# Kernel optimization log

Measured on AMD Instinct MI355X. Metric: run time of the kernel, lower is better.

## Reference

```python
import jax, jax.numpy as jnp
import numpy as np
from jax import lax

N_CHANNELS = 64
N_FILTERS = 256
N_LAYERS = 9  # residual blocks use dilations 2**1 .. 2**(N_LAYERS-1)


def causal_conv1d(x, w, dilation):
    """Causal dilated conv. x: [B,T,Cin], w: [K,Cin,Cout]."""
    pad = (w.shape[0] - 1) * dilation
    return lax.conv_general_dilated(
        x, w, window_strides=(1,), padding=[(pad, 0)],
        rhs_dilation=(dilation,), dimension_numbers=("NWC", "WIO", "NWC"))


def setup_inputs() -> dict:
    key = jax.random.key(0)
    ks = jax.random.split(key, 12)
    B, T, C, F, L = 8, 4096, N_CHANNELS, N_FILTERS, N_LAYERS
    s = lambda fan_in: 1.0 / np.sqrt(fan_in)
    return {
        "x": jax.random.normal(ks[0], (B, T, C), jnp.float32),
        "Wc": jax.random.normal(ks[1], (2, C, F), jnp.float32) * s(2 * C),
        "Wf": jax.random.normal(ks[2], (L - 1, 2, F, F), jnp.float32) * s(2 * F),
        "Wg": jax.random.normal(ks[3], (L - 1, 2, F, F), jnp.float32) * s(2 * F),
        "Wr": jax.random.normal(ks[4], (L - 1, F, F), jnp.float32) * s(F),
        "br": jnp.zeros((L - 1, F), jnp.float32),
        "Ws": jax.random.normal(ks[5], (L - 1, F, F), jnp.float32) * s(F),
        "bs": jnp.zeros((L - 1, F), jnp.float32),
        "Wd1": jax.random.normal(ks[6], (F, C), jnp.float32) * s(F),
        "bd1": jnp.zeros((C,), jnp.float32),
        "Wd2": jax.random.normal(ks[7], (C, C), jnp.float32) * s(C),
        "bd2": jnp.zeros((C,), jnp.float32),
    }


def reference(x, Wc, Wf, Wg, Wr, br, Ws, bs, Wd1, bd1, Wd2, bd2):
    # Initial causal conv, dilation 1, no bias.
    out = causal_conv1d(x, Wc, 1)  # [B,T,F]
    skip_sum = jnp.zeros_like(out)
    for i in range(N_LAYERS - 1):
        d = 2 ** (i + 1)
        f = causal_conv1d(out, Wf[i], d)
        g = causal_conv1d(out, Wg[i], d)
        z = jnp.tanh(f) * jax.nn.sigmoid(g)
        out = out + jnp.einsum("btf,fo->bto", z, Wr[i]) + br[i]
        skip_sum = skip_sum + jnp.einsum("btf,fo->bto", z, Ws[i]) + bs[i]
    h = jax.nn.selu(skip_sum)
    h = jnp.einsum("btf,fc->btc", h, Wd1) + bd1
    h = jax.nn.selu(h)
    h = jnp.einsum("btc,co->bto", h, Wd2) + bd2
    return h
```

## Files before the change

### kernel.cpp

```cpp
#include <hip/hip_runtime.h>
#include <cstdint>

typedef unsigned short u16;
typedef unsigned int u32;
typedef __attribute__((ext_vector_type(8))) short s8v;
typedef __attribute__((ext_vector_type(4))) float f4v;

#define FCH 256

__device__ __forceinline__ float bf2f(u16 u){ return __uint_as_float(((u32)u)<<16); }
__device__ __forceinline__ u16 f2bf(float x){
  u32 u = __float_as_uint(x);
  u += 0x7fffu + ((u>>16)&1u);
  return (u16)(u>>16);
}
__device__ __forceinline__ uint4 pack8(float4 a, float4 b){
  uint4 o;
  o.x = (u32)f2bf(a.x) | ((u32)f2bf(a.y)<<16);
  o.y = (u32)f2bf(a.z) | ((u32)f2bf(a.w)<<16);
  o.z = (u32)f2bf(b.x) | ((u32)f2bf(b.y)<<16);
  o.w = (u32)f2bf(b.z) | ((u32)f2bf(b.w)<<16);
  return o;
}
__device__ __forceinline__ float seluf(float x){
  const float sc = 1.0507009873554805f, al = 1.6732632423543772f;
  return x > 0.f ? sc*x : sc*al*(__expf(x)-1.f);
}
__device__ __forceinline__ int xcd_tile(int bid, int nT8){
  return nT8 ? ((bid & 7) * nT8 + (bid >> 3)) : bid;
}

__global__ __launch_bounds__(256) void pack_kernel(
    const float* __restrict__ Wc, const float* __restrict__ Wf, const float* __restrict__ Wg,
    const float* __restrict__ Wr, const float* __restrict__ Ws,
    const float* __restrict__ Wd1, const float* __restrict__ Wd2,
    u16* __restrict__ Bp1, u16* __restrict__ Bp2, u16* __restrict__ Bp0,
    u16* __restrict__ BpD1, u16* __restrict__ BpD2)
{
  int gid = blockIdx.x*256 + threadIdx.x;
  int frag = gid >> 6;
  int lane = gid & 63;
  int q = lane >> 4, i15 = lane & 15;
  u16 v[8];
  u16* dst;
  if (frag < 4096) {
    int layer = frag >> 9, rem = frag & 511;
    int kc = rem >> 5, nt = rem & 31;
    int n = nt*16 + i15;
    const float* W = (n < 256) ? Wf : Wg;
    int nn = (n < 256) ? n : n - 256;
    #pragma unroll
    for (int j = 0; j < 8; ++j) {
      int k = kc*32 + q*8 + j;
      int tap = k >> 8, cin = k & 255;
      v[j] = f2bf(W[((size_t)((layer*2 + tap)*256 + cin))*256 + nn]);
    }
    dst = Bp1 + (size_t)frag*512 + lane*8;
  } else if (frag < 6144) {
    int f = frag - 4096;
    int layer = f >> 8, rem = f & 255;
    int kc = rem >> 5, nt = rem & 31;
    int n = nt*16 + i15;
    const float* W = (n < 256) ? Wr : Ws;
    int nn = (n < 256) ? n : n - 256;
    #pragma unroll
    for (int j = 0; j < 8; ++j) {
      int k = kc*32 + q*8 + j;
      v[j] = f2bf(W[((size_t)(layer*256 + k))*256 + nn]);
    }
    dst = Bp2 + (size_t)f*512 + lane*8;
  } else if (frag < 6208) {
    int f = frag - 6144;
    int kc = f >> 4, nt = f & 15;
    int n = nt*16 + i15;
    #pragma unroll
    for (int j = 0; j < 8; ++j) {
      int k = kc*32 + q*8 + j;
      int tap = k >> 6, cin = k & 63;
      v[j] = f2bf(Wc[(size_t)(tap*64 + cin)*256 + n]);
    }
    dst = Bp0 + (size_t)f*512 + lane*8;
  } else if (frag < 6240) {
    int f = frag - 6208;
    int kc = f >> 2, nt = f & 3;
    int n = nt*16 + i15;
    #pragma unroll
    for (int j = 0; j < 8; ++j) {
      int k = kc*32 + q*8 + j;
      v[j] = f2bf(Wd1[(size_t)k*64 + n]);
    }
    dst = BpD1 + (size_t)f*512 + lane*8;
  } else if (frag < 6248) {
    int f = frag - 6240;
    int kc = f >> 2, nt = f & 3;
    int n = nt*16 + i15;
    #pragma unroll
    for (int j = 0; j < 8; ++j) {
      int k = kc*32 + q*8 + j;
      v[j] = f2bf(Wd2[(size_t)k*64 + n]);
    }
    dst = BpD2 + (size_t)f*512 + lane*8;
  } else return;
  uint4 o;
  o.x = (u32)v[0] | ((u32)v[1] << 16);
  o.y = (u32)v[2] | ((u32)v[3] << 16);
  o.z = (u32)v[4] | ((u32)v[5] << 16);
  o.w = (u32)v[6] | ((u32)v[7] << 16);
  *reinterpret_cast<uint4*>(dst) = o;
}

__global__ __launch_bounds__(256, 2) void conv0_kernel(
    const float* __restrict__ x, u16* __restrict__ outBf,
    const u16* __restrict__ Bp0, int nT8)
{
  __shared__ __align__(16) u16 ldsA[2][2048];
  const int tid = threadIdx.x;
  const int w = tid >> 6, lane = tid & 63, q = lane >> 4, i15 = lane & 15;
  const int rb = xcd_tile(blockIdx.x, nT8) * 64;
  const int sm = tid >> 2, sg = tid & 3;
  const int grow = rb + sm;
  const int tpos = grow & 4095;
  const int sunit = ((sm >> 4)*64 + sg*16 + ((sm & 15) ^ (sg << 1))) * 8;
  const int runit = (q*16 + (i15 ^ (q << 1))) * 8;

  f4v acc[4][4];
  #pragma unroll
  for (int jj = 0; jj < 4; ++jj)
    #pragma unroll
    for (int mt = 0; mt < 4; ++mt)
      acc[jj][mt] = (f4v){0.f,0.f,0.f,0.f};

  float4 f0 = {0.f,0.f,0.f,0.f}, f1 = {0.f,0.f,0.f,0.f};
  if (tpos >= 1) {
    const float* px = x + (size_t)(grow-1)*64 + sg*8;
    f0 = *reinterpret_cast<const float4*>(px);
    f1 = *reinterpret_cast<const float4*>(px + 4);
  }
  *reinterpret_cast<uint4*>(&ldsA[0][sunit]) = pack8(f0, f1);
  s8v bcur[4], bnxt[4];
  #pragma unroll
  for (int jj = 0; jj < 4; ++jj)
    bcur[jj] = *reinterpret_cast<const s8v*>(Bp0 + ((size_t)(w + 4*jj)*64 + lane)*8);
  __syncthreads();

  for (int kc = 0; kc < 4; ++kc) {
    const int cur = kc & 1;
    uint4 an = {0u,0u,0u,0u};
    if (kc < 3) {
      int kg = (kc+1)*32 + sg*8;
      int tap = kg >> 6, col = kg & 63;
      float4 g0 = {0.f,0.f,0.f,0.f}, g1 = {0.f,0.f,0.f,0.f};
      if (tap) {
        const float* px = x + (size_t)grow*64 + col;
        g0 = *reinterpret_cast<const float4*>(px);
        g1 = *reinterpret_cast<const float4*>(px + 4);
      } else if (tpos >= 1) {
        const float* px = x + (size_t)(grow-1)*64 + col;
        g0 = *reinterpret_cast<const float4*>(px);
        g1 = *reinterpret_cast<const float4*>(px + 4);
      }
      an = pack8(g0, g1);
      #pragma unroll
      for (int jj = 0; jj < 4; ++jj)
        bnxt[jj] = *reinterpret_cast<const s8v*>(Bp0 + (((size_t)(kc+1)*16 + (w + 4*jj))*64 + lane)*8);
    }
    s8v af[4];
    #pragma unroll
    for (int mt = 0; mt < 4; ++mt)
      af[mt] = *reinterpret_cast<const s8v*>(&ldsA[cur][mt*512 + runit]);
    #pragma unroll
    for (int jj = 0; jj < 4; ++jj)
      #pragma unroll
      for (int mt = 0; mt < 4; ++mt)
        acc[jj][mt] = __builtin_amdgcn_mfma_f32_16x16x32_bf16(af[mt], bcur[jj], acc[jj][mt], 0,0,0);
    if (kc < 3) {
      *reinterpret_cast<uint4*>(&ldsA[cur ^ 1][sunit]) = an;
      #pragma unroll
      for (int jj = 0; jj < 4; ++jj) bcur[jj] = bnxt[jj];
    }
    __syncthreads();
  }

  #pragma unroll
  for (int jj = 0; jj < 4; ++jj) {
    const int cc = (w + 4*jj)*16 + i15;
    #pragma unroll
    for (int mt = 0; mt < 4; ++mt)
      #pragma unroll
      for (int r = 0; r < 4; ++r) {
        const int g2 = rb + mt*16 + q*4 + r;
        outBf[(size_t)g2*FCH + cc] = f2bf(acc[jj][mt][r]);
      }
  }
}

__global__ __launch_bounds__(256, 3) void layer_kernel(
    const u16* __restrict__ inBf, u16* __restrict__ outBf,
    u16* __restrict__ skipB,
    const u16* __restrict__ Bp1, const u16* __restrict__ Bp2,
    const float* __restrict__ br, const float* __restrict__ bs,
    int dil, int first, int nT8)
{
  __shared__ __align__(16) u16 ldsA[2][32*40];
  __shared__ __align__(16) u16 ldsZ[32*264];
  const int tid = threadIdx.x;
  const int w = tid >> 6, lane = tid & 63, q = lane >> 4, i15 = lane & 15;
  const int rb = xcd_tile(blockIdx.x, nT8) * 32;
  const int sm = tid >> 3, sg = tid & 7;
  const int grow = rb + sm;
  const int tpos = grow & 4095;

  f4v acc[8][2];
  #pragma unroll
  for (int jj = 0; jj < 8; ++jj)
    #pragma unroll
    for (int mt = 0; mt < 2; ++mt)
      acc[jj][mt] = (f4v){0.f,0.f,0.f,0.f};

  {
    uint2 a0 = {0u,0u};
    if (tpos >= dil)
      a0 = *reinterpret_cast<const uint2*>(inBf + (size_t)(grow - dil)*FCH + sg*4);
    *reinterpret_cast<uint2*>(&ldsA[0][sm*40 + sg*4]) = a0;
    s8v bcur[8], bnxt[8];
    #pragma unroll
    for (int jj = 0; jj < 8; ++jj)
      bcur[jj] = *reinterpret_cast<const s8v*>(Bp1 + ((size_t)(w + 4*jj)*64 + lane)*8);
    __syncthreads();

    for (int kc = 0; kc < 16; ++kc) {
      const int cur = kc & 1;
      uint2 an = {0u,0u};
      if (kc < 15) {
        int kg = (kc+1)*32 + sg*4;
        int tap = kg >> 8, col = kg & 255;
        if (tap) an = *reinterpret_cast<const uint2*>(inBf + (size_t)grow*FCH + col);
        else if (tpos >= dil) an = *reinterpret_cast<const uint2*>(inBf + (size_t)(grow - dil)*FCH + col);
        #pragma unroll
        for (int jj = 0; jj < 8; ++jj)
          bnxt[jj] = *reinterpret_cast<const s8v*>(Bp1 + (((size_t)(kc+1)*32 + (w + 4*jj))*64 + lane)*8);
      }
      s8v af[2];
      #pragma unroll
      for (int mt = 0; mt < 2; ++mt)
        af[mt] = *reinterpret_cast<const s8v*>(&ldsA[cur][(mt*16 + i15)*40 + q*8]);
      #pragma unroll
      for (int jj = 0; jj < 8; ++jj)
        #pragma unroll
        for (int mt = 0; mt < 2; ++mt)
          acc[jj][mt] = __builtin_amdgcn_mfma_f32_16x16x32_bf16(af[mt], bcur[jj], acc[jj][mt], 0,0,0);
      if (kc < 15) {
        *reinterpret_cast<uint2*>(&ldsA[cur ^ 1][sm*40 + sg*4]) = an;
        #pragma unroll
        for (int jj = 0; jj < 8; ++jj) bcur[jj] = bnxt[jj];
      }
      __syncthreads();
    }
  }

  #pragma unroll
  for (int jj = 0; jj < 4; ++jj) {
    const int colb = (w + 4*jj)*16 + i15;
    #pragma unroll
    for (int mt = 0; mt < 2; ++mt)
      #pragma unroll
      for (int r = 0; r < 4; ++r) {
        float f = acc[jj][mt][r];
        float g = acc[jj+4][mt][r];
        float z = (1.f - 2.f/(__expf(2.f*f) + 1.f)) * (1.f/(1.f + __expf(-g)));
        ldsZ[(mt*16 + q*4 + r)*264 + colb] = f2bf(z);
      }
  }
  __syncthreads();

  #pragma unroll
  for (int jj = 0; jj < 8; ++jj) {
    const int nt = w + 4*jj;
    const bool isR = (jj < 4);
    const int cc = (isR ? nt*16 : (nt-16)*16) + i15;
    const float bias = isR ? br[cc] : bs[cc];
    #pragma unroll
    for (int mt = 0; mt < 2; ++mt)
      #pragma unroll
      for (int r = 0; r < 4; ++r) {
        const int g2 = rb + mt*16 + q*4 + r;
        float vv;
        if (isR) vv = bf2f(inBf[(size_t)g2*FCH + cc]) + bias;
        else     vv = first ? bias : (bf2f(skipB[(size_t)g2*FCH + cc]) + bias);
        acc[jj][mt][r] = vv;
      }
  }

  {
    s8v b2c[8], b2n[8];
    #pragma unroll
    for (int jj = 0; jj < 8; ++jj)
      b2c[jj] = *reinterpret_cast<const s8v*>(Bp2 + ((size_t)(w + 4*jj)*64 + lane)*8);
    for (int kc = 0; kc < 8; ++kc) {
      if (kc < 7) {
        #pragma unroll
        for (int jj = 0; jj < 8; ++jj)
          b2n[jj] = *reinterpret_cast<const s8v*>(Bp2 + (((size_t)(kc+1)*32 + (w + 4*jj))*64 + lane)*8);
      }
      s8v af[2];
      #pragma unroll
      for (int mt = 0; mt < 2; ++mt)
        af[mt] = *reinterpret_cast<const s8v*>(&ldsZ[(mt*16 + i15)*264 + kc*32 + q*8]);
      #pragma unroll
      for (int jj = 0; jj < 8; ++jj)
        #pragma unroll
        for (int mt = 0; mt < 2; ++mt)
          acc[jj][mt] = __builtin_amdgcn_mfma_f32_16x16x32_bf16(af[mt], b2c[jj], acc[jj][mt], 0,0,0);
      if (kc < 7) {
        #pragma unroll
        for (int jj = 0; jj < 8; ++jj) b2c[jj] = b2n[jj];
      }
    }
  }

  #pragma unroll
  for (int jj = 0; jj < 8; ++jj) {
    const int nt = w + 4*jj;
    const bool isR = (jj < 4);
    const int cc = (isR ? nt*16 : (nt-16)*16) + i15;
    #pragma unroll
    for (int mt = 0; mt < 2; ++mt)
      #pragma unroll
      for (int r = 0; r < 4; ++r) {
        const int g2 = rb + mt*16 + q*4 + r;
        u16 hv = f2bf(acc[jj][mt][r]);
        if (isR) outBf[(size_t)g2*FCH + cc] = hv;
        else     skipB[(size_t)g2*FCH + cc] = hv;
      }
  }
}

__global__ __launch_bounds__(256, 2) void final_kernel(
    const u16* __restrict__ skipB, const u16* __restrict__ BpD1, const u16* __restrict__ BpD2,
    const float* __restrict__ bd1, const float* __restrict__ bd2, float* __restrict__ outp,
    int nT8)
{
  __shared__ __align__(16) u16 ldsH[64*264];
  __shared__ __align__(16) u16 ldsH2[64*72];
  const int tid = threadIdx.x;
  const int w = tid >> 6, lane = tid & 63, q = lane >> 4, i15 = lane & 15;
  const int rb = xcd_tile(blockIdx.x, nT8) * 64;
  const int sm = tid >> 2, sseg = tid & 3;

  {
    const u16* sp = skipB + (size_t)(rb + sm)*256 + sseg*64;
    u16* dr = &ldsH[sm*264 + sseg*64];
    #pragma unroll
    for (int u = 0; u < 8; ++u) {
      uint4 raw = *reinterpret_cast<const uint4*>(sp + u*8);
      u32 rr[4] = {raw.x, raw.y, raw.z, raw.w};
      uint4 o;
      u32 oo[4];
      #pragma unroll
      for (int p = 0; p < 4; ++p) {
        float e0 = seluf(bf2f((u16)(rr[p] & 0xffffu)));
        float e1 = seluf(bf2f((u16)(rr[p] >> 16)));
        oo[p] = (u32)f2bf(e0) | ((u32)f2bf(e1) << 16);
      }
      o.x = oo[0]; o.y = oo[1]; o.z = oo[2]; o.w = oo[3];
      *reinterpret_cast<uint4*>(dr + u*8) = o;
    }
  }
  __syncthreads();

  f4v a1[4];
  #pragma unroll
  for (int mt = 0; mt < 4; ++mt) a1[mt] = (f4v){0.f,0.f,0.f,0.f};
  for (int kc = 0; kc < 8; ++kc) {
    s8v b = *reinterpret_cast<const s8v*>(BpD1 + ((size_t)(kc*4 + w)*64 + lane)*8);
    #pragma unroll
    for (int mt = 0; mt < 4; ++mt) {
      s8v af = *reinterpret_cast<const s8v*>(&ldsH[(mt*16 + i15)*264 + kc*32 + q*8]);
      a1[mt] = __builtin_amdgcn_mfma_f32_16x16x32_bf16(af, b, a1[mt], 0,0,0);
    }
  }
  const float bb1 = bd1[w*16 + i15];
  #pragma unroll
  for (int mt = 0; mt < 4; ++mt)
    #pragma unroll
    for (int r = 0; r < 4; ++r)
      ldsH2[(mt*16 + q*4 + r)*72 + w*16 + i15] = f2bf(seluf(a1[mt][r] + bb1));
  __syncthreads();

  f4v a2[4];
  #pragma unroll
  for (int mt = 0; mt < 4; ++mt) a2[mt] = (f4v){0.f,0.f,0.f,0.f};
  #pragma unroll
  for (int kc = 0; kc < 2; ++kc) {
    s8v b = *reinterpret_cast<const s8v*>(BpD2 + ((size_t)(kc*4 + w)*64 + lane)*8);
    #pragma unroll
    for (int mt = 0; mt < 4; ++mt) {
      s8v af = *reinterpret_cast<const s8v*>(&ldsH2[(mt*16 + i15)*72 + kc*32 + q*8]);
      a2[mt] = __builtin_amdgcn_mfma_f32_16x16x32_bf16(af, b, a2[mt], 0,0,0);
    }
  }
  const float bb2 = bd2[w*16 + i15];
  #pragma unroll
  for (int mt = 0; mt < 4; ++mt)
    #pragma unroll
    for (int r = 0; r < 4; ++r)
      outp[(size_t)(rb + mt*16 + q*4 + r)*64 + w*16 + i15] = a2[mt][r] + bb2;
}

__global__ __launch_bounds__(256) void zero_kernel(uint4* __restrict__ outp, int n16)
{
  int i = blockIdx.x*256 + threadIdx.x;
  if (i < n16) outp[i] = (uint4){0u,0u,0u,0u};
}

extern "C" void kernel_launch(void* const* d_in, const int* in_sizes, int n_in,
                              void* d_out, int out_size, void* d_ws, size_t ws_size,
                              hipStream_t stream)
{
  (void)n_in;
  const float* x   = (const float*)d_in[0];
  const float* Wc  = (const float*)d_in[1];
  const float* Wf  = (const float*)d_in[2];
  const float* Wg  = (const float*)d_in[3];
  const float* Wr  = (const float*)d_in[4];
  const float* br  = (const float*)d_in[5];
  const float* Ws  = (const float*)d_in[6];
  const float* bs  = (const float*)d_in[7];
  const float* Wd1 = (const float*)d_in[8];
  const float* bd1 = (const float*)d_in[9];
  const float* Wd2 = (const float*)d_in[10];
  const float* bd2 = (const float*)d_in[11];

  const size_t ROWS = (size_t)in_sizes[0] / 64;
  const int gridC = (int)(ROWS / 64);
  const int gridL = (int)(ROWS / 32);
  const int nT8C = (gridC % 8 == 0) ? gridC / 8 : 0;
  const int nT8L = (gridL % 8 == 0) ? gridL / 8 : 0;

  const size_t packsB = (size_t)6248 * 512 * 2;
  const size_t bfBuf  = ROWS * 256 * 2;
  const size_t needB = packsB + 3*bfBuf;

  if (ws_size < needB) {
    int n16 = (out_size * 4) / 16;
    zero_kernel<<<(n16 + 255)/256, 256, 0, stream>>>((uint4*)d_out, n16);
    return;
  }

  char* ws = (char*)d_ws;
  u16* Bp1    = (u16*)ws;            ws += (size_t)4096*512*2;
  u16* Bp2    = (u16*)ws;            ws += (size_t)2048*512*2;
  u16* Bp0    = (u16*)ws;            ws += (size_t)64*512*2;
  u16* BpD1   = (u16*)ws;            ws += (size_t)32*512*2;
  u16* BpD2   = (u16*)ws;            ws += (size_t)8*512*2;
  u16* skipB  = (u16*)ws;            ws += bfBuf;
  u16* bufA   = (u16*)ws;            ws += bfBuf;
  u16* bufB   = (u16*)ws;            ws += bfBuf;

  pack_kernel<<<1562, 256, 0, stream>>>(Wc, Wf, Wg, Wr, Ws, Wd1, Wd2,
                                        Bp1, Bp2, Bp0, BpD1, BpD2);
  conv0_kernel<<<gridC, 256, 0, stream>>>(x, bufA, Bp0, nT8C);
  u16* bufs[2] = {bufA, bufB};
  for (int i = 0; i < 8; ++i) {
    layer_kernel<<<gridL, 256, 0, stream>>>(
        bufs[i & 1], bufs[(i + 1) & 1], skipB,
        Bp1 + (size_t)i*262144, Bp2 + (size_t)i*131072,
        br + i*256, bs + i*256, 2 << i, (i == 0) ? 1 : 0, nT8L);
  }
  final_kernel<<<gridC, 256, 0, stream>>>(skipB, BpD1, BpD2, bd1, bd2,
                                          (float*)d_out, nT8C);
}
```

Before: 594.3 us.

## Load dilated-conv A fragments directly from global, drop LDS staging and barriers

The first GEMM in layer_kernel no longer stages the activation tile through double-buffered shared memory with a barrier every k-step. Each lane now reads its MFMA A fragment straight from global memory (the shifted tap first, then the current tap), and a zero fragment is used when the row is before the dilation. Both GEMM loops also drop the explicit register double-buffering of weight fragments and load each B fragment just before use, leaving the overlap to unroll-by-2 and the compiler. This removes the LDS traffic and per-step syncs and lowers register pressure, but the global A loads become less coalesced and B load latency may be less well hidden.

New measurement: 889.5 us. 49.7% more time.

```diff
diff --git a/kernel.cpp b/kernel.cpp
--- a/kernel.cpp
+++ b/kernel.cpp
@@ -201,14 +201,10 @@
     const float* __restrict__ br, const float* __restrict__ bs,
     int dil, int first, int nT8)
 {
-  __shared__ __align__(16) u16 ldsA[2][32*40];
   __shared__ __align__(16) u16 ldsZ[32*264];
   const int tid = threadIdx.x;
   const int w = tid >> 6, lane = tid & 63, q = lane >> 4, i15 = lane & 15;
   const int rb = xcd_tile(blockIdx.x, nT8) * 32;
-  const int sm = tid >> 3, sg = tid & 7;
-  const int grow = rb + sm;
-  const int tpos = grow & 4095;
 
   f4v acc[8][2];
   #pragma unroll
@@ -218,43 +214,45 @@
       acc[jj][mt] = (f4v){0.f,0.f,0.f,0.f};
 
   {
-    uint2 a0 = {0u,0u};
-    if (tpos >= dil)
-      a0 = *reinterpret_cast<const uint2*>(inBf + (size_t)(grow - dil)*FCH + sg*4);
-    *reinterpret_cast<uint2*>(&ldsA[0][sm*40 + sg*4]) = a0;
-    s8v bcur[8], bnxt[8];
-    #pragma unroll
-    for (int jj = 0; jj < 8; ++jj)
-      bcur[jj] = *reinterpret_cast<const s8v*>(Bp1 + ((size_t)(w + 4*jj)*64 + lane)*8);
-    __syncthreads();
-
-    for (int kc = 0; kc < 16; ++kc) {
-      const int cur = kc & 1;
-      uint2 an = {0u,0u};
-      if (kc < 15) {
-        int kg = (kc+1)*32 + sg*4;
-        int tap = kg >> 8, col = kg & 255;
-        if (tap) an = *reinterpret_cast<const uint2*>(inBf + (size_t)grow*FCH + col);
-        else if (tpos >= dil) an = *reinterpret_cast<const uint2*>(inBf + (size_t)(grow - dil)*FCH + col);
-        #pragma unroll
-        for (int jj = 0; jj < 8; ++jj)
-          bnxt[jj] = *reinterpret_cast<const s8v*>(Bp1 + (((size_t)(kc+1)*32 + (w + 4*jj))*64 + lane)*8);
-      }
+    const u16* aptr0[2];
+    const u16* aptr1[2];
+    bool vld[2];
+    #pragma unroll
+    for (int mt = 0; mt < 2; ++mt) {
+      const int row = rb + mt*16 + i15;
+      vld[mt]   = (row & 4095) >= dil;
+      aptr0[mt] = inBf + (size_t)(row - dil)*FCH + q*8;
+      aptr1[mt] = inBf + (size_t)row*FCH + q*8;
+    }
+    const s8v zz = {0,0,0,0,0,0,0,0};
+
+    #pragma unroll 2
+    for (int kc = 0; kc < 8; ++kc) {
       s8v af[2];
       #pragma unroll
       for (int mt = 0; mt < 2; ++mt)
-        af[mt] = *reinterpret_cast<const s8v*>(&ldsA[cur][(mt*16 + i15)*40 + q*8]);
-      #pragma unroll
-      for (int jj = 0; jj < 8; ++jj)
+        af[mt] = vld[mt] ? *reinterpret_cast<const s8v*>(aptr0[mt] + kc*32) : zz;
+      #pragma unroll
+      for (int jj = 0; jj < 8; ++jj) {
+        s8v b = *reinterpret_cast<const s8v*>(Bp1 + (((size_t)kc*32 + (w + 4*jj))*64 + lane)*8);
         #pragma unroll
         for (int mt = 0; mt < 2; ++mt)
-          acc[jj][mt] = __builtin_amdgcn_mfma_f32_16x16x32_bf16(af[mt], bcur[jj], acc[jj][mt], 0,0,0);
-      if (kc < 15) {
-        *reinterpret_cast<uint2*>(&ldsA[cur ^ 1][sm*40 + sg*4]) = an;
+          acc[jj][mt] = __builtin_amdgcn_mfma_f32_16x16x32_bf16(af[mt], b, acc[jj][mt], 0,0,0);
+      }
+    }
+    #pragma unroll 2
+    for (int kc = 8; kc < 16; ++kc) {
+      s8v af[2];
+      #pragma unroll
+      for (int mt = 0; mt < 2; ++mt)
+        af[mt] = *reinterpret_cast<const s8v*>(aptr1[mt] + (kc - 8)*32);
+      #pragma unroll
+      for (int jj = 0; jj < 8; ++jj) {
+        s8v b = *reinterpret_cast<const s8v*>(Bp1 + (((size_t)kc*32 + (w + 4*jj))*64 + lane)*8);
         #pragma unroll
-        for (int jj = 0; jj < 8; ++jj) bcur[jj] = bnxt[jj];
-      }
-      __syncthreads();
+        for (int mt = 0; mt < 2; ++mt)
+          acc[jj][mt] = __builtin_amdgcn_mfma_f32_16x16x32_bf16(af[mt], b, acc[jj][mt], 0,0,0);
+      }
     }
   }
 
@@ -292,28 +290,18 @@
   }
 
   {
-    s8v b2c[8], b2n[8];
-    #pragma unroll
-    for (int jj = 0; jj < 8; ++jj)
-      b2c[jj] = *reinterpret_cast<const s8v*>(Bp2 + ((size_t)(w + 4*jj)*64 + lane)*8);
+    #pragma unroll 2
     for (int kc = 0; kc < 8; ++kc) {
-      if (kc < 7) {
-        #pragma unroll
-        for (int jj = 0; jj < 8; ++jj)
-          b2n[jj] = *reinterpret_cast<const s8v*>(Bp2 + (((size_t)(kc+1)*32 + (w + 4*jj))*64 + lane)*8);
-      }
       s8v af[2];
       #pragma unroll
       for (int mt = 0; mt < 2; ++mt)
         af[mt] = *reinterpret_cast<const s8v*>(&ldsZ[(mt*16 + i15)*264 + kc*32 + q*8]);
       #pragma unroll
-      for (int jj = 0; jj < 8; ++jj)
+      for (int jj = 0; jj < 8; ++jj) {
+        s8v b = *reinterpret_cast<const s8v*>(Bp2 + (((size_t)kc*32 + (w + 4*jj))*64 + lane)*8);
         #pragma unroll
         for (int mt = 0; mt < 2; ++mt)
-          acc[jj][mt] = __builtin_amdgcn_mfma_f32_16x16x32_bf16(af[mt], b2c[jj], acc[jj][mt], 0,0,0);
-      if (kc < 7) {
-        #pragma unroll
-        for (int jj = 0; jj < 8; ++jj) b2c[jj] = b2n[jj];
+          acc[jj][mt] = __builtin_amdgcn_mfma_f32_16x16x32_bf16(af[mt], b, acc[jj][mt], 0,0,0);
       }
     }
   }
```

## Load dilated-conv A fragments directly from global memory and drop LDS staging

Applied to the files above, without the earlier changes.

The first GEMM in the layer kernel now loads each MFMA A fragment straight from global memory into registers, with a mask that zeroes causal-padding rows. This removes the double-buffered LDS tile and the per-k-step __syncthreads. The second GEMM prefetches its first B fragments and the next LDS Z fragments in software. The residual and skip loads are moved after the GEMM and added in the epilogue, with accumulators starting from zero. These changes cut barriers and LDS traffic, at the cost of redundant global loads across waves and more registers held live.

Measured after the change: 542.6 us. -8.7%, faster.

```diff
diff --git a/kernel.cpp b/kernel.cpp
--- a/kernel.cpp
+++ b/kernel.cpp
@@ -25,6 +25,12 @@
 __device__ __forceinline__ float seluf(float x){
   const float sc = 1.0507009873554805f, al = 1.6732632423543772f;
   return x > 0.f ? sc*x : sc*al*(__expf(x)-1.f);
+}
+__device__ __forceinline__ s8v ldmask(const u16* p, u32 m){
+  uint4 r = *reinterpret_cast<const uint4*>(p);
+  r.x &= m; r.y &= m; r.z &= m; r.w &= m;
+  s8v v; *reinterpret_cast<uint4*>(&v) = r;
+  return v;
 }
 __device__ __forceinline__ int xcd_tile(int bid, int nT8){
   return nT8 ? ((bid & 7) * nT8 + (bid >> 3)) : bid;
@@ -201,14 +207,10 @@
     const float* __restrict__ br, const float* __restrict__ bs,
     int dil, int first, int nT8)
 {
-  __shared__ __align__(16) u16 ldsA[2][32*40];
   __shared__ __align__(16) u16 ldsZ[32*264];
   const int tid = threadIdx.x;
   const int w = tid >> 6, lane = tid & 63, q = lane >> 4, i15 = lane & 15;
   const int rb = xcd_tile(blockIdx.x, nT8) * 32;
-  const int sm = tid >> 3, sg = tid & 7;
-  const int grow = rb + sm;
-  const int tpos = grow & 4095;
 
   f4v acc[8][2];
   #pragma unroll
@@ -218,45 +220,58 @@
       acc[jj][mt] = (f4v){0.f,0.f,0.f,0.f};
 
   {
-    uint2 a0 = {0u,0u};
-    if (tpos >= dil)
-      a0 = *reinterpret_cast<const uint2*>(inBf + (size_t)(grow - dil)*FCH + sg*4);
-    *reinterpret_cast<uint2*>(&ldsA[0][sm*40 + sg*4]) = a0;
-    s8v bcur[8], bnxt[8];
+    const u16* a0p[2];
+    const u16* a1p[2];
+    u32 am[2];
+    #pragma unroll
+    for (int mt = 0; mt < 2; ++mt) {
+      const int row = rb + mt*16 + i15;
+      const bool v = (row & 4095) >= dil;
+      a0p[mt] = inBf + (size_t)(v ? row - dil : row)*FCH + q*8;
+      a1p[mt] = inBf + (size_t)row*FCH + q*8;
+      am[mt]  = v ? 0xffffffffu : 0u;
+    }
+
+    s8v bcur[8], bnxt[8], afc[2], afn[2];
     #pragma unroll
     for (int jj = 0; jj < 8; ++jj)
       bcur[jj] = *reinterpret_cast<const s8v*>(Bp1 + ((size_t)(w + 4*jj)*64 + lane)*8);
-    __syncthreads();
-
+    #pragma unroll
+    for (int mt = 0; mt < 2; ++mt)
+      afc[mt] = ldmask(a0p[mt], am[mt]);
+
+    #pragma unroll 2
     for (int kc = 0; kc < 16; ++kc) {
-      const int cur = kc & 1;
-      uint2 an = {0u,0u};
-      if (kc < 15) {
-        int kg = (kc+1)*32 + sg*4;
-        int tap = kg >> 8, col = kg & 255;
-        if (tap) an = *reinterpret_cast<const uint2*>(inBf + (size_t)grow*FCH + col);
-        else if (tpos >= dil) an = *reinterpret_cast<const uint2*>(inBf + (size_t)(grow - dil)*FCH + col);
+      const int kn = kc + 1;
+      if (kn < 16) {
         #pragma unroll
         for (int jj = 0; jj < 8; ++jj)
-          bnxt[jj] = *reinterpret_cast<const s8v*>(Bp1 + (((size_t)(kc+1)*32 + (w + 4*jj))*64 + lane)*8);
-      }
-      s8v af[2];
-      #pragma unroll
-      for (int mt = 0; mt < 2; ++mt)
-        af[mt] = *reinterpret_cast<const s8v*>(&ldsA[cur][(mt*16 + i15)*40 + q*8]);
+          bnxt[jj] = *reinterpret_cast<const s8v*>(Bp1 + (((size_t)kn*32 + (w + 4*jj))*64 + lane)*8);
+        if (kn < 8) {
+          #pragma unroll
+          for (int mt = 0; mt < 2; ++mt)
+            afn[mt] = ldmask(a0p[mt] + kn*32, am[mt]);
+        } else {
+          #pragma unroll
+          for (int mt = 0; mt < 2; ++mt)
+            afn[mt] = *reinterpret_cast<const s8v*>(a1p[mt] + (kn - 8)*32);
+        }
+      }
       #pragma unroll
       for (int jj = 0; jj < 8; ++jj)
         #pragma unroll
         for (int mt = 0; mt < 2; ++mt)
-          acc[jj][mt] = __builtin_amdgcn_mfma_f32_16x16x32_bf16(af[mt], bcur[jj], acc[jj][mt], 0,0,0);
-      if (kc < 15) {
-        *reinterpret_cast<uint2*>(&ldsA[cur ^ 1][sm*40 + sg*4]) = an;
-        #pragma unroll
-        for (int jj = 0; jj < 8; ++jj) bcur[jj] = bnxt[jj];
-      }
-      __syncthreads();
-    }
-  }
+          acc[jj][mt] = __builtin_amdgcn_mfma_f32_16x16x32_bf16(afc[mt], bcur[jj], acc[jj][mt], 0,0,0);
+      #pragma unroll
+      for (int jj = 0; jj < 8; ++jj) bcur[jj] = bnxt[jj];
+      afc[0] = afn[0]; afc[1] = afn[1];
+    }
+  }
+
+  s8v b2c[8], b2n[8];
+  #pragma unroll
+  for (int jj = 0; jj < 8; ++jj)
+    b2c[jj] = *reinterpret_cast<const s8v*>(Bp2 + ((size_t)(w + 4*jj)*64 + lane)*8);
 
   #pragma unroll
   for (int jj = 0; jj < 4; ++jj) {
@@ -271,8 +286,61 @@
         ldsZ[(mt*16 + q*4 + r)*264 + colb] = f2bf(z);
       }
   }
+  #pragma unroll
+  for (int jj = 0; jj < 8; ++jj)
+    #pragma unroll
+    for (int mt = 0; mt < 2; ++mt)
+      acc[jj][mt] = (f4v){0.f,0.f,0.f,0.f};
   __syncthreads();
 
+  {
+    s8v zfc[2], zfn[2];
+    #pragma unroll
+    for (int mt = 0; mt < 2; ++mt)
+      zfc[mt] = *reinterpret_cast<const s8v*>(&ldsZ[(mt*16 + i15)*264 + q*8]);
+    #pragma unroll 2
+    for (int kc = 0; kc < 8; ++kc) {
+      const int kn = kc + 1;
+      if (kn < 8) {
+        #pragma unroll
+        for (int jj = 0; jj < 8; ++jj)
+          b2n[jj] = *reinterpret_cast<const s8v*>(Bp2 + (((size_t)kn*32 + (w + 4*jj))*64 + lane)*8);
+        #pragma unroll
+        for (int mt = 0; mt < 2; ++mt)
+          zfn[mt] = *reinterpret_cast<const s8v*>(&ldsZ[(mt*16 + i15)*264 + kn*32 + q*8]);
+      }
+      #pragma unroll
+      for (int jj = 0; jj < 8; ++jj)
+        #pragma unroll
+        for (int mt = 0; mt < 2; ++mt)
+          acc[jj][mt] = __builtin_amdgcn_mfma_f32_16x16x32_bf16(zfc[mt], b2c[jj], acc[jj][mt], 0,0,0);
+      #pragma unroll
+      for (int jj = 0; jj < 8; ++jj) b2c[jj] = b2n[jj];
+      zfc[0] = zfn[0]; zfc[1] = zfn[1];
+    }
+  }
+
+  u16 resv[4][2][4], skv[4][2][4];
+  #pragma unroll
+  for (int jj = 0; jj < 4; ++jj) {
+    const int cc = (w + 4*jj)*16 + i15;
+    #pragma unroll
+    for (int mt = 0; mt < 2; ++mt)
+      #pragma unroll
+      for (int r = 0; r < 4; ++r)
+        resv[jj][mt][r] = inBf[(size_t)(rb + mt*16 + q*4 + r)*FCH + cc];
+  }
+  if (!first) {
+    #pragma unroll
+    for (int jj = 0; jj < 4; ++jj) {
+      const int cc = (w + 4*jj)*16 + i15;
+      #pragma unroll
+      for (int mt = 0; mt < 2; ++mt)
+        #pragma unroll
+        for (int r = 0; r < 4; ++r)
+          skv[jj][mt][r] = skipB[(size_t)(rb + mt*16 + q*4 + r)*FCH + cc];
+    }
+  }
   #pragma unroll
   for (int jj = 0; jj < 8; ++jj) {
     const int nt = w + 4*jj;
@@ -284,51 +352,10 @@
       #pragma unroll
       for (int r = 0; r < 4; ++r) {
         const int g2 = rb + mt*16 + q*4 + r;
-        float vv;
-        if (isR) vv = bf2f(inBf[(size_t)g2*FCH + cc]) + bias;
-        else     vv = first ? bias : (bf2f(skipB[(size_t)g2*FCH + cc]) + bias);
-        acc[jj][mt][r] = vv;
-      }
-  }
-
-  {
-    s8v b2c[8], b2n[8];
-    #pragma unroll
-    for (int jj = 0; jj < 8; ++jj)
-      b2c[jj] = *reinterpret_cast<const s8v*>(Bp2 + ((size_t)(w + 4*jj)*64 + lane)*8);
-    for (int kc = 0; kc < 8; ++kc) {
-      if (kc < 7) {
-        #pragma unroll
-        for (int jj = 0; jj < 8; ++jj)
-          b2n[jj] = *reinterpret_cast<const s8v*>(Bp2 + (((size_t)(kc+1)*32 + (w + 4*jj))*64 + lane)*8);
-      }
-      s8v af[2];
-      #pragma unroll
-      for (int mt = 0; mt < 2; ++mt)
-        af[mt] = *reinterpret_cast<const s8v*>(&ldsZ[(mt*16 + i15)*264 + kc*32 + q*8]);
-      #pragma unroll
-      for (int jj = 0; jj < 8; ++jj)
-        #pragma unroll
-        for (int mt = 0; mt < 2; ++mt)
-          acc[jj][mt] = __builtin_amdgcn_mfma_f32_16x16x32_bf16(af[mt], b2c[jj], acc[jj][mt], 0,0,0);
-      if (kc < 7) {
-        #pragma unroll
-        for (int jj = 0; jj < 8; ++jj) b2c[jj] = b2n[jj];
-      }
-    }
-  }
-
-  #pragma unroll
-  for (int jj = 0; jj < 8; ++jj) {
-    const int nt = w + 4*jj;
-    const bool isR = (jj < 4);
-    const int cc = (isR ? nt*16 : (nt-16)*16) + i15;
-    #pragma unroll
-    for (int mt = 0; mt < 2; ++mt)
-      #pragma unroll
-      for (int r = 0; r < 4; ++r) {
-        const int g2 = rb + mt*16 + q*4 + r;
-        u16 hv = f2bf(acc[jj][mt][r]);
+        float vv = acc[jj][mt][r] + bias;
+        if (isR) vv += bf2f(resv[jj][mt][r]);
+        else if (!first) vv += bf2f(skv[jj-4][mt][r]);
+        u16 hv = f2bf(vv);
         if (isR) outBf[(size_t)g2*FCH + cc] = hv;
         else     skipB[(size_t)g2*FCH + cc] = hv;
       }
```
